# Performance work log

Hardware: AMD Instinct MI355X
Metric: run time of the kernel (lower is better)

## Reference

```python
import jax, jax.numpy as jnp
import numpy as np

B, NCROPS, T = 512, 5, 8192
NEG = -1e30  # masked fill for invalid (beyond-seqlen) positions


def setup_inputs() -> dict:
    key = jax.random.key(0)
    k1, k2, k3 = jax.random.split(key, 3)
    scores = jax.random.normal(k1, (B * NCROPS, T), dtype=jnp.float32)
    label = jax.random.randint(k2, (B,), 0, 2, dtype=jnp.int32)
    # valid lengths in [16, T] so that k = seqlen//16 + 1 is always in range
    seqlen = jax.random.randint(k3, (B,), 16, T + 1, dtype=jnp.int32)
    return {"scores": scores, "label": label, "seqlen": seqlen}


def reference(scores, label, seqlen):
    # uncrop 'mean': [B*ncrops, T] -> [B, T]
    s = scores.reshape(B, NCROPS, T).mean(axis=1)

    # mask invalid positions, sort each row descending (vectorized ragged top-k)
    valid = jnp.arange(T)[None, :] < seqlen[:, None]            # [B, T]
    s_sorted = -jnp.sort(-jnp.where(valid, s, NEG), axis=1)     # descending
    csum = jnp.cumsum(s_sorted, axis=1)                         # [B, T]

    # get_k: label==0 -> 1; k==-1 -> seqlen//16 + 1 (k-1 < seqlen always)
    k = jnp.where(label == 0, 1, seqlen // 16 + 1)              # [B]
    topk_sum = jnp.take_along_axis(csum, (k - 1)[:, None], axis=1)[:, 0]
    vl_scores = topk_sum / k.astype(s.dtype)                    # mean of top-k

    # BCEWithLogitsLoss (mean reduction): logaddexp(0, v) - v*y
    y = label.astype(s.dtype)
    loss = jnp.mean(jnp.logaddexp(0.0, vl_scores) - vl_scores * y)
    return loss
```

## Files before the change

kernel.cpp:

```cpp
#include <hip/hip_runtime.h>
#include <stdint.h>

#define BB      512
#define NCROPS  5
#define TT      8192
#define THREADS 512
#define WAVES   8
#define HPAD    257

__device__ __forceinline__ uint32_t f2ord(float f) {
    uint32_t b = __float_as_uint(f);
    return (b & 0x80000000u) ? ~b : (b | 0x80000000u);
}
__device__ __forceinline__ float ord2f(uint32_t u) {
    uint32_t b = (u & 0x80000000u) ? (u & 0x7FFFFFFFu) : ~u;
    return __uint_as_float(b);
}

#define FOR4(OP) OP(u0) OP(u1) OP(u2) OP(u3)

#define LOADJ(BASE, SL, A0,A1,A2,A3,A4, J, PRED) \
    const bool PRED = (4 * (tid + (J) * THREADS) < (SL)); \
    float4 A0, A1, A2, A3, A4; \
    if (PRED) { \
        const int t4 = tid + (J) * THREADS; \
        A0 = *reinterpret_cast<const float4*>((BASE) + 0 * TT + 4 * t4); \
        A1 = *reinterpret_cast<const float4*>((BASE) + 1 * TT + 4 * t4); \
        A2 = *reinterpret_cast<const float4*>((BASE) + 2 * TT + 4 * t4); \
        A3 = *reinterpret_cast<const float4*>((BASE) + 3 * TT + 4 * t4); \
        A4 = *reinterpret_cast<const float4*>((BASE) + 4 * TT + 4 * t4); \
    }

#define KEYJ(DST, SL, A0,A1,A2,A3,A4, J, PRED) \
    if (PRED) { \
        const int t0 = 4 * (tid + (J) * THREADS); \
        float4 m; \
        m.x = (A0.x + A1.x + A2.x + A3.x + A4.x) * 0.2f; \
        m.y = (A0.y + A1.y + A2.y + A3.y + A4.y) * 0.2f; \
        m.z = (A0.z + A1.z + A2.z + A3.z + A4.z) * 0.2f; \
        m.w = (A0.w + A1.w + A2.w + A3.w + A4.w) * 0.2f; \
        DST.x = f2ord(m.x); \
        DST.y = (t0 + 1 < (SL)) ? f2ord(m.y) : 0u; \
        DST.z = (t0 + 2 < (SL)) ? f2ord(m.z) : 0u; \
        DST.w = (t0 + 3 < (SL)) ? f2ord(m.w) : 0u; \
    } else { DST.x = 0u; DST.y = 0u; DST.z = 0u; DST.w = 0u; }

#define MAXOP(V) mx = max(mx, max(max(V.x, V.y), max(V.z, V.w)));
#define H0(X)    if ((X) != 0u) atomicAdd(&h[(X) >> 24], 1u);
#define H0V(V)   H0(V.x) H0(V.y) H0(V.z) H0(V.w)
#define HR(X)    if ((X) != 0u && ((X) >> shp) == p) atomicAdd(&h[((X) >> shd) & 255u], 1u);
#define HRV(V)   HR(V.x) HR(V.y) HR(V.z) HR(V.w)

#define SELECT(THR, KK) { \
    if ((KK) == 1) { \
        uint32_t mx = 0u; \
        FOR4(MAXOP) \
        for (int off = 32; off; off >>= 1) { \
            const uint32_t o = (uint32_t)__shfl_down((int)mx, off); \
            mx = max(mx, o); \
        } \
        if (lane == 0) s_m[wave] = mx; \
        __syncthreads(); \
        uint32_t rowmax = s_m[0]; \
        for (int w = 1; w < WAVES; ++w) rowmax = max(rowmax, s_m[w]); \
        THR = rowmax; \
    } else { \
        uint32_t p = 0u, kr = (uint32_t)(KK); \
        for (int r = 0; r < 4; ++r) { \
            uint32_t* h = &hist[r & 1][wave][0]; \
            if (r == 0) { FOR4(H0V) } \
            else { \
                const int shp = 32 - 8 * r; \
                const int shd = shp - 8; \
                FOR4(HRV) \
            } \
            __syncthreads(); \
            if (wave == 0) { \
                uint32_t t0s = 0u, t1s = 0u, t2s = 0u, t3s = 0u; \
                for (int w = 0; w < WAVES; ++w) { \
                    const uint32_t* hw = &hist[r & 1][w][0]; \
                    t0s += hw[4 * lane + 0]; \
                    t1s += hw[4 * lane + 1]; \
                    t2s += hw[4 * lane + 2]; \
                    t3s += hw[4 * lane + 3]; \
                } \
                const uint32_t s = t0s + t1s + t2s + t3s; \
                uint32_t suf = s; \
                for (int off = 1; off < 64; off <<= 1) { \
                    const uint32_t v = (uint32_t)__shfl_down((int)suf, off); \
                    if (lane + off < 64) suf += v; \
                } \
                const uint32_t E  = suf - s; \
                const uint32_t T3 = E  + t3s; \
                const uint32_t T2 = T3 + t2s; \
                const uint32_t T1 = T2 + t1s; \
                const uint32_t T0 = T1 + t0s; \
                const unsigned long long bal = __ballot(T0 >= kr); \
                const int L = 63 - __clzll(bal); \
                if (lane == L) { \
                    uint32_t j, Tj, tj; \
                    if      (T3 >= kr) { j = 3u; Tj = T3; tj = t3s; } \
                    else if (T2 >= kr) { j = 2u; Tj = T2; tj = t2s; } \
                    else if (T1 >= kr) { j = 1u; Tj = T1; tj = t1s; } \
                    else               { j = 0u; Tj = T0; tj = t0s; } \
                    bc_p = (p << 8) | (uint32_t)(4 * lane) | j; \
                    bc_k = kr - (Tj - tj); \
                } \
            } else { \
                 \
                uint32_t* hz = &hist[(r + 1) & 1][0][0]; \
                for (int i = tid - 64; i < WAVES * HPAD; i += (THREADS - 64)) hz[i] = 0u; \
            } \
            __syncthreads(); \
            p  = bc_p; \
            kr = bc_k; \
        } \
        THR = p; \
    } }

#define SUMOP(V) \
    if (V.x >= _thr) { sg += ord2f(V.x); cg++; } \
    if (V.y >= _thr) { sg += ord2f(V.y); cg++; } \
    if (V.z >= _thr) { sg += ord2f(V.z); cg++; } \
    if (V.w >= _thr) { sg += ord2f(V.w); cg++; }

#define EPILOGUE(THR, KK, LB, ROW) { \
    const uint32_t _thr = (THR); \
    float sg = 0.f; int cg = 0; \
    FOR4(SUMOP) \
    for (int off = 32; off; off >>= 1) { \
        sg += __shfl_down(sg, off); \
        cg += __shfl_down(cg, off); \
    } \
    if (lane == 0) { s_s[wave] = sg; s_c[wave] = cg; } \
    __syncthreads(); \
    if (tid == 0) { \
        float S = 0.f; int C = 0; \
        for (int w = 0; w < WAVES; ++w) { S += s_s[w]; C += s_c[w]; } \
        const float kf   = ord2f(_thr); \
        const float topk = S - (float)(C - (KK)) * kf; \
        const float v    = topk / (float)(KK); \
        const float y    = (float)(LB); \
        const float la   = fmaxf(v, 0.f) + log1pf(expf(-fabsf(v))); \
        row_loss[ROW] = la - v * y; \
    } }

__global__ __launch_bounds__(THREADS, 2) void topk_loss_pairs(
    const float* __restrict__ scores, const int* __restrict__ label,
    const int* __restrict__ seqlen, float* __restrict__ row_loss)
{
    const int tid  = threadIdx.x;
    const int lane = tid & 63;
    const int wave = tid >> 6;
    const int rA   = blockIdx.x;
    const int rB   = blockIdx.x + 256;

    const int slA = seqlen[rA], lbA = label[rA];
    const int slB = seqlen[rB], lbB = label[rB];
    const int kA  = (lbA == 0) ? 1 : (slA / 16 + 1);
    const int kB  = (lbB == 0) ? 1 : (slB / 16 + 1);

    __shared__ uint32_t hist[2][WAVES][HPAD];
    __shared__ uint32_t bc_p, bc_k;
    __shared__ uint32_t s_m[WAVES];
    __shared__ float    s_s[WAVES];
    __shared__ int      s_c[WAVES];
    __shared__ uint32_t s_pad[17000];
    if (slA == -2147483647) s_pad[tid] = 0u;

    const float* baseA = scores + (size_t)rA * NCROPS * TT;
    const float* baseB = scores + (size_t)rB * NCROPS * TT;

    LOADJ(baseA, slA, a0,a1,a2,a3,a4, 0, pa0)
    LOADJ(baseA, slA, b0,b1,b2,b3,b4, 1, pa1)
    LOADJ(baseA, slA, c0,c1,c2,c3,c4, 2, pa2)
    LOADJ(baseA, slA, d0,d1,d2,d3,d4, 3, pa3)

    {
        uint32_t* hz = &hist[0][0][0];
        for (int i = tid; i < WAVES * HPAD; i += THREADS) hz[i] = 0u;
    }
    __syncthreads();

    uint4 u0, u1, u2, u3;
    KEYJ(u0, slA, a0,a1,a2,a3,a4, 0, pa0)
    KEYJ(u1, slA, b0,b1,b2,b3,b4, 1, pa1)
    KEYJ(u2, slA, c0,c1,c2,c3,c4, 2, pa2)
    KEYJ(u3, slA, d0,d1,d2,d3,d4, 3, pa3)

    LOADJ(baseB, slB, e0,e1,e2,e3,e4, 0, pb0)
    LOADJ(baseB, slB, f0,f1,f2,f3,f4, 1, pb1)
    LOADJ(baseB, slB, g0,g1,g2,g3,g4, 2, pb2)
    LOADJ(baseB, slB, h0,h1,h2,h3,h4, 3, pb3)

    uint32_t thrA;
    SELECT(thrA, kA)
    EPILOGUE(thrA, kA, lbA, rA)

    KEYJ(u0, slB, e0,e1,e2,e3,e4, 0, pb0)
    KEYJ(u1, slB, f0,f1,f2,f3,f4, 1, pb1)
    KEYJ(u2, slB, g0,g1,g2,g3,g4, 2, pb2)
    KEYJ(u3, slB, h0,h1,h2,h3,h4, 3, pb3)

    uint32_t thrB;
    SELECT(thrB, kB)
    EPILOGUE(thrB, kB, lbB, rB)
}

__global__ __launch_bounds__(256) void reduce_loss(
    const float* __restrict__ row_loss, float* __restrict__ out)
{
    const int tid = threadIdx.x;
    float v = row_loss[tid] + row_loss[tid + 256];
    #pragma unroll
    for (int off = 32; off; off >>= 1) v += __shfl_down(v, off);
    __shared__ float s[4];
    if ((tid & 63) == 0) s[tid >> 6] = v;
    __syncthreads();
    if (tid == 0) out[0] = (s[0] + s[1] + s[2] + s[3]) * (1.0f / 512.0f);
}

extern "C" void kernel_launch(void* const* d_in, const int* in_sizes, int n_in,
                              void* d_out, int out_size, void* d_ws, size_t ws_size,
                              hipStream_t stream) {
    const float* scores = (const float*)d_in[0];
    const int*   label  = (const int*)d_in[1];
    const int*   seqlen = (const int*)d_in[2];
    float* out      = (float*)d_out;
    float* row_loss = (float*)d_ws;

    topk_loss_pairs<<<BB / 2, THREADS, 0, stream>>>(scores, label, seqlen, row_loss);
    reduce_loss<<<1, 256, 0, stream>>>(row_loss, out);
}
```

Baseline: 26.95 us.

## Use atomic work queue for row scheduling and fuse final loss reduction

Rows are no longer assigned to blocks as fixed pairs. Each of the 256 persistent blocks pulls row indices from a global atomic counter, and the next row's loads are prefetched while the current row goes through selection. The last block to finish, detected with a done counter, computes the mean loss, which removes the second kernel launch. The large shared-memory padding array is also dropped. In exchange the launch path adds a memset, and each row adds extra barriers and an atomic round trip.

After: 36.46 us. 1.35x slower.

```diff
diff --git a/kernel.cpp b/kernel.cpp
--- a/kernel.cpp
+++ b/kernel.cpp
@@ -6,6 +6,7 @@
 #define TT      8192
 #define THREADS 512
 #define WAVES   8
+#define NBLK    256
 #define HPAD    257
 
 __device__ __forceinline__ uint32_t f2ord(float f) {
@@ -19,31 +20,42 @@
 
 #define FOR4(OP) OP(u0) OP(u1) OP(u2) OP(u3)
 
-#define LOADJ(BASE, SL, A0,A1,A2,A3,A4, J, PRED) \
-    const bool PRED = (4 * (tid + (J) * THREADS) < (SL)); \
-    float4 A0, A1, A2, A3, A4; \
-    if (PRED) { \
-        const int t4 = tid + (J) * THREADS; \
-        A0 = *reinterpret_cast<const float4*>((BASE) + 0 * TT + 4 * t4); \
-        A1 = *reinterpret_cast<const float4*>((BASE) + 1 * TT + 4 * t4); \
-        A2 = *reinterpret_cast<const float4*>((BASE) + 2 * TT + 4 * t4); \
-        A3 = *reinterpret_cast<const float4*>((BASE) + 3 * TT + 4 * t4); \
-        A4 = *reinterpret_cast<const float4*>((BASE) + 4 * TT + 4 * t4); \
-    }
-
-#define KEYJ(DST, SL, A0,A1,A2,A3,A4, J, PRED) \
-    if (PRED) { \
-        const int t0 = 4 * (tid + (J) * THREADS); \
-        float4 m; \
-        m.x = (A0.x + A1.x + A2.x + A3.x + A4.x) * 0.2f; \
-        m.y = (A0.y + A1.y + A2.y + A3.y + A4.y) * 0.2f; \
-        m.z = (A0.z + A1.z + A2.z + A3.z + A4.z) * 0.2f; \
-        m.w = (A0.w + A1.w + A2.w + A3.w + A4.w) * 0.2f; \
-        DST.x = f2ord(m.x); \
-        DST.y = (t0 + 1 < (SL)) ? f2ord(m.y) : 0u; \
-        DST.z = (t0 + 2 < (SL)) ? f2ord(m.z) : 0u; \
-        DST.w = (t0 + 3 < (SL)) ? f2ord(m.w) : 0u; \
+#define ISSUE1(BASE, SL, A,B,C,D,E, J) \
+    if (4 * (tid + (J) * THREADS) < (SL)) { \
+        const float* bp_ = (BASE) + 4 * (tid + (J) * THREADS); \
+        A = *reinterpret_cast<const float4*>(bp_); \
+        B = *reinterpret_cast<const float4*>(bp_ + 1 * TT); \
+        C = *reinterpret_cast<const float4*>(bp_ + 2 * TT); \
+        D = *reinterpret_cast<const float4*>(bp_ + 3 * TT); \
+        E = *reinterpret_cast<const float4*>(bp_ + 4 * TT); \
+    }
+
+#define ISSUE(ROW, SL) { \
+    const float* base_ = scores + (size_t)(ROW) * (NCROPS * TT); \
+    ISSUE1(base_, SL, a0,a1,a2,a3,a4, 0) \
+    ISSUE1(base_, SL, b0,b1,b2,b3,b4, 1) \
+    ISSUE1(base_, SL, c0,c1,c2,c3,c4, 2) \
+    ISSUE1(base_, SL, d0,d1,d2,d3,d4, 3) }
+
+#define KEY1(DST, SL, A,B,C,D,E, J) \
+    if (4 * (tid + (J) * THREADS) < (SL)) { \
+        const int t0_ = 4 * (tid + (J) * THREADS); \
+        float4 m_; \
+        m_.x = (A.x + B.x + C.x + D.x + E.x) * 0.2f; \
+        m_.y = (A.y + B.y + C.y + D.y + E.y) * 0.2f; \
+        m_.z = (A.z + B.z + C.z + D.z + E.z) * 0.2f; \
+        m_.w = (A.w + B.w + C.w + D.w + E.w) * 0.2f; \
+        DST.x = f2ord(m_.x); \
+        DST.y = (t0_ + 1 < (SL)) ? f2ord(m_.y) : 0u; \
+        DST.z = (t0_ + 2 < (SL)) ? f2ord(m_.z) : 0u; \
+        DST.w = (t0_ + 3 < (SL)) ? f2ord(m_.w) : 0u; \
     } else { DST.x = 0u; DST.y = 0u; DST.z = 0u; DST.w = 0u; }
+
+#define KEYS(SL) \
+    KEY1(u0, SL, a0,a1,a2,a3,a4, 0) \
+    KEY1(u1, SL, b0,b1,b2,b3,b4, 1) \
+    KEY1(u2, SL, c0,c1,c2,c3,c4, 2) \
+    KEY1(u3, SL, d0,d1,d2,d3,d4, 3)
 
 #define MAXOP(V) mx = max(mx, max(max(V.x, V.y), max(V.z, V.w)));
 #define H0(X)    if ((X) != 0u) atomicAdd(&h[(X) >> 24], 1u);
@@ -107,7 +119,6 @@
                     bc_k = kr - (Tj - tj); \
                 } \
             } else { \
-                 \
                 uint32_t* hz = &hist[(r + 1) & 1][0][0]; \
                 for (int i = tid - 64; i < WAVES * HPAD; i += (THREADS - 64)) hz[i] = 0u; \
             } \
@@ -143,81 +154,89 @@
         const float y    = (float)(LB); \
         const float la   = fmaxf(v, 0.f) + log1pf(expf(-fabsf(v))); \
         row_loss[ROW] = la - v * y; \
-    } }
-
-__global__ __launch_bounds__(THREADS, 2) void topk_loss_pairs(
+    } \
+    __syncthreads(); }
+
+__global__ __launch_bounds__(THREADS, 2) void queue_topk(
     const float* __restrict__ scores, const int* __restrict__ label,
-    const int* __restrict__ seqlen, float* __restrict__ row_loss)
+    const int* __restrict__ seqlen, float* __restrict__ row_loss,
+    uint32_t* __restrict__ qctr, uint32_t* __restrict__ done,
+    float* __restrict__ out)
 {
     const int tid  = threadIdx.x;
     const int lane = tid & 63;
     const int wave = tid >> 6;
-    const int rA   = blockIdx.x;
-    const int rB   = blockIdx.x + 256;
-
-    const int slA = seqlen[rA], lbA = label[rA];
-    const int slB = seqlen[rB], lbB = label[rB];
-    const int kA  = (lbA == 0) ? 1 : (slA / 16 + 1);
-    const int kB  = (lbB == 0) ? 1 : (slB / 16 + 1);
 
     __shared__ uint32_t hist[2][WAVES][HPAD];
     __shared__ uint32_t bc_p, bc_k;
     __shared__ uint32_t s_m[WAVES];
     __shared__ float    s_s[WAVES];
     __shared__ int      s_c[WAVES];
-    __shared__ uint32_t s_pad[17000];
-    if (slA == -2147483647) s_pad[tid] = 0u;
-
-    const float* baseA = scores + (size_t)rA * NCROPS * TT;
-    const float* baseB = scores + (size_t)rB * NCROPS * TT;
-
-    LOADJ(baseA, slA, a0,a1,a2,a3,a4, 0, pa0)
-    LOADJ(baseA, slA, b0,b1,b2,b3,b4, 1, pa1)
-    LOADJ(baseA, slA, c0,c1,c2,c3,c4, 2, pa2)
-    LOADJ(baseA, slA, d0,d1,d2,d3,d4, 3, pa3)
+    __shared__ int      s_next;
+    __shared__ int      s_go;
 
     {
         uint32_t* hz = &hist[0][0][0];
         for (int i = tid; i < WAVES * HPAD; i += THREADS) hz[i] = 0u;
     }
+
+    float4 a0,a1,a2,a3,a4, b0,b1,b2,b3,b4, c0,c1,c2,c3,c4, d0,d1,d2,d3,d4;
+
     __syncthreads();
-
-    uint4 u0, u1, u2, u3;
-    KEYJ(u0, slA, a0,a1,a2,a3,a4, 0, pa0)
-    KEYJ(u1, slA, b0,b1,b2,b3,b4, 1, pa1)
-    KEYJ(u2, slA, c0,c1,c2,c3,c4, 2, pa2)
-    KEYJ(u3, slA, d0,d1,d2,d3,d4, 3, pa3)
-
-    LOADJ(baseB, slB, e0,e1,e2,e3,e4, 0, pb0)
-    LOADJ(baseB, slB, f0,f1,f2,f3,f4, 1, pb1)
-    LOADJ(baseB, slB, g0,g1,g2,g3,g4, 2, pb2)
-    LOADJ(baseB, slB, h0,h1,h2,h3,h4, 3, pb3)
-
-    uint32_t thrA;
-    SELECT(thrA, kA)
-    EPILOGUE(thrA, kA, lbA, rA)
-
-    KEYJ(u0, slB, e0,e1,e2,e3,e4, 0, pb0)
-    KEYJ(u1, slB, f0,f1,f2,f3,f4, 1, pb1)
-    KEYJ(u2, slB, g0,g1,g2,g3,g4, 2, pb2)
-    KEYJ(u3, slB, h0,h1,h2,h3,h4, 3, pb3)
-
-    uint32_t thrB;
-    SELECT(thrB, kB)
-    EPILOGUE(thrB, kB, lbB, rB)
-}
-
-__global__ __launch_bounds__(256) void reduce_loss(
-    const float* __restrict__ row_loss, float* __restrict__ out)
-{
-    const int tid = threadIdx.x;
-    float v = row_loss[tid] + row_loss[tid + 256];
-    #pragma unroll
-    for (int off = 32; off; off >>= 1) v += __shfl_down(v, off);
-    __shared__ float s[4];
-    if ((tid & 63) == 0) s[tid >> 6] = v;
+    if (tid == 0) s_next = (int)atomicAdd(qctr, 1u);
     __syncthreads();
-    if (tid == 0) out[0] = (s[0] + s[1] + s[2] + s[3]) * (1.0f / 512.0f);
+    int cur = s_next;
+    int slc = 0;
+    if (cur < BB) {
+        slc = seqlen[cur];
+        ISSUE(cur, slc)
+    }
+
+    while (cur < BB) {
+        uint4 u0, u1, u2, u3;
+        KEYS(slc)
+        const int lb = label[cur];
+        const int k  = (lb == 0) ? 1 : (slc / 16 + 1);
+
+        __syncthreads();
+        if (tid == 0) s_next = (int)atomicAdd(qctr, 1u);
+        __syncthreads();
+        const int nxt = s_next;
+        int sln = 0;
+        if (nxt < BB) {
+            sln = seqlen[nxt];
+            ISSUE(nxt, sln)
+        }
+        asm volatile("" ::: "memory");
+
+        uint32_t thr;
+        SELECT(thr, k)
+        EPILOGUE(thr, k, lb, cur)
+
+        cur = nxt;
+        slc = sln;
+    }
+
+    if (tid == 0) {
+        __threadfence();
+        s_go = (atomicAdd(done, 1u) == (uint32_t)(NBLK - 1));
+    }
+    __syncthreads();
+    if (s_go) {
+        __threadfence();
+        float v = __hip_atomic_load(&row_loss[tid], __ATOMIC_RELAXED,
+                                    __HIP_MEMORY_SCOPE_AGENT);
+        #pragma unroll
+        for (int off = 32; off; off >>= 1) v += __shfl_down(v, off);
+        if (lane == 0) s_s[wave] = v;
+        __syncthreads();
+        if (tid == 0) {
+            float S = 0.f;
+            #pragma unroll
+            for (int w = 0; w < WAVES; ++w) S += s_s[w];
+            out[0] = S * (1.0f / (float)BB);
+        }
+    }
 }
 
 extern "C" void kernel_launch(void* const* d_in, const int* in_sizes, int n_in,
@@ -226,9 +245,13 @@
     const float* scores = (const float*)d_in[0];
     const int*   label  = (const int*)d_in[1];
     const int*   seqlen = (const int*)d_in[2];
-    float* out      = (float*)d_out;
-    float* row_loss = (float*)d_ws;
-
-    topk_loss_pairs<<<BB / 2, THREADS, 0, stream>>>(scores, label, seqlen, row_loss);
-    reduce_loss<<<1, 256, 0, stream>>>(row_loss, out);
-}
+    float* out = (float*)d_out;
+
+    float*    row_loss = (float*)d_ws;
+    uint32_t* qctr     = (uint32_t*)((char*)d_ws + 2048);
+    uint32_t* done     = qctr + 1;
+
+    hipMemsetAsync(qctr, 0, 2 * sizeof(uint32_t), stream);
+    queue_topk<<<NBLK, THREADS, 0, stream>>>(scores, label, seqlen,
+                                             row_loss, qctr, done, out);
+}
```
